# Optimization experiments

Measured on AMD Instinct MI355X. Metric: run time of the kernel, lower is better.

Reference implementation:

```python
import jax, jax.numpy as jnp
import numpy as np

N_HEADS = 16
CONTEXT_WINDOW = 256


def _band_mask(s_q, s_k):
    # True = masked out. Module (causal=True, context_window=256) allows only
    # keys with 0 <= (query_pos - key_pos) < CONTEXT_WINDOW (causal mask is
    # subsumed by the lower band).
    d = jnp.arange(s_q)[:, None] - jnp.arange(s_k)[None, :]
    return ~((d >= 0) & (d < CONTEXT_WINDOW))


def setup_inputs() -> dict:
    key = jax.random.key(0)
    ks = jax.random.split(key, 5)
    B, S, D = 2, 2048, 1024
    std = 0.02
    return {
        "query": jax.random.normal(ks[0], (B, S, D), dtype=jnp.float32),
        "Wq": jax.random.normal(ks[1], (D, D), dtype=jnp.float32) * std,
        "bq": jnp.zeros((D,), dtype=jnp.float32),
        "Wk": jax.random.normal(ks[2], (D, D), dtype=jnp.float32) * std,
        "bk": jnp.zeros((D,), dtype=jnp.float32),
        "Wv": jax.random.normal(ks[3], (D, D), dtype=jnp.float32) * std,
        "bv": jnp.zeros((D,), dtype=jnp.float32),
        "Wo": jax.random.normal(ks[4], (D, D), dtype=jnp.float32) * std,
        "bo": jnp.zeros((D,), dtype=jnp.float32),
    }


def reference(query, Wq, bq, Wk, bk, Wv, bv, Wo, bo):
    B, S, D = query.shape
    H = N_HEADS
    Dh = D // H
    # projections -> [B, H, S, Dh]
    q = (query @ Wq + bq).reshape(B, S, H, Dh).transpose(0, 2, 1, 3)
    k = (query @ Wk + bk).reshape(B, S, H, Dh).transpose(0, 2, 1, 3)
    v = (query @ Wv + bv).reshape(B, S, H, Dh).transpose(0, 2, 1, 3)
    scores = jnp.einsum("bhqd,bhkd->bhqk", q, k) * (1.0 / np.sqrt(Dh))
    mask = _band_mask(S, S)  # [S, S]
    scores = jnp.where(mask[None, None, :, :], -jnp.inf, scores)
    attn = jax.nn.softmax(scores, axis=-1)
    out = jnp.einsum("bhqk,bhkd->bhqd", attn, v)
    out = out.transpose(0, 2, 1, 3).reshape(B, S, D)
    return out @ Wo + bo
```

## Files before the change

kernel.cpp:

```cpp
#include <hip/hip_runtime.h>
#include <hip/hip_bf16.h>


typedef __bf16 bf16x8 __attribute__((ext_vector_type(8)));
typedef float f32x4 __attribute__((ext_vector_type(4)));
typedef short s16x4 __attribute__((ext_vector_type(4)));
typedef unsigned short u16x8 __attribute__((ext_vector_type(8)));
typedef unsigned short u16x4 __attribute__((ext_vector_type(4)));

__device__ __forceinline__ unsigned short f2bf(float f) {
  unsigned int u = __builtin_bit_cast(unsigned int, f);
  u += 0x7FFFu + ((u >> 16) & 1u);
  return (unsigned short)(u >> 16);
}

__device__ __forceinline__ f32x4 mfma32(bf16x8 a, bf16x8 b, f32x4 c) {
  return __builtin_amdgcn_mfma_f32_16x16x32_bf16(a, b, c, 0, 0, 0);
}
__device__ __forceinline__ f32x4 mfma16(s16x4 a, s16x4 b, f32x4 c) {
  return __builtin_amdgcn_mfma_f32_16x16x16bf16_1k(a, b, c, 0, 0, 0);
}

__device__ __forceinline__ void gl16(const unsigned short* gsrc,
                                     unsigned short* lds) {
  __builtin_amdgcn_global_load_lds(
      (const __attribute__((address_space(1))) unsigned int*)gsrc,
      (__attribute__((address_space(3))) unsigned int*)lds, 16, 0, 0);
}

__global__ __launch_bounds__(256) void cvt_all(
    const float* __restrict__ x,
    const float* __restrict__ Wq, const float* __restrict__ Wk,
    const float* __restrict__ Wv, const float* __restrict__ Wo,
    unsigned short* __restrict__ xb, unsigned short* __restrict__ Wt) {
  const int z = blockIdx.z;
  const int tx = threadIdx.x, ty = threadIdx.y;
  if (z == 4) {
    const int tid = (blockIdx.y * 32 + blockIdx.x) * 256 + ty * 32 + tx;
#pragma unroll
    for (int it = 0; it < 4; ++it) {
      const int i = tid + it * 262144;
      const float4 v = ((const float4*)x)[i];
      u16x4 o = { f2bf(v.x), f2bf(v.y), f2bf(v.z), f2bf(v.w) };
      *(u16x4*)(xb + (size_t)i * 4) = o;
    }
    return;
  }
  const float* W = (z == 0) ? Wq : (z == 1) ? Wk : (z == 2) ? Wv : Wo;
  unsigned short* dst = Wt + (size_t)z * 1024 * 1024;
  __shared__ float t[32][33];
  const int n0 = blockIdx.x * 32, k0 = blockIdx.y * 32;
#pragma unroll
  for (int i = 0; i < 32; i += 8)
    t[ty + i][tx] = W[(size_t)(k0 + ty + i) * 1024 + n0 + tx];
  __syncthreads();
#pragma unroll
  for (int i = 0; i < 32; i += 8)
    dst[(size_t)(n0 + ty + i) * 1024 + k0 + tx] = f2bf(t[tx][ty + i]);
}

__global__ __launch_bounds__(256) void gemm_qkv(
    const unsigned short* __restrict__ A, const unsigned short* __restrict__ Bt,
    const float* __restrict__ bq, const float* __restrict__ bk,
    const float* __restrict__ bv,
    unsigned short* __restrict__ q_ws, unsigned short* __restrict__ k_ws,
    unsigned short* __restrict__ v_ws) {
  __shared__ unsigned short Alds[128 * 32];
  __shared__ unsigned short Blds[128 * 32];
  const int tid = threadIdx.x, lane = tid & 63, w = tid >> 6;
  const int lq = lane & 15, lg = lane >> 4;
  const int bm = blockIdx.x, bn = blockIdx.y;
  const int wr = (w >> 1) * 64, wc = (w & 1) * 64;

  const int srow = lane >> 2, scol8 = (lane & 3) * 8;
  const unsigned short* Ag =
      A + (size_t)(bm * 128 + w * 32 + srow) * 1024 + scol8;
  const unsigned short* Bg =
      Bt + (size_t)(bn * 128 + w * 32 + srow) * 1024 + scol8;
  unsigned short* Al0 = Alds + (w * 32) * 32;
  unsigned short* Al1 = Alds + (w * 32 + 16) * 32;
  unsigned short* Bl0 = Blds + (w * 32) * 32;
  unsigned short* Bl1 = Blds + (w * 32 + 16) * 32;

  f32x4 acc[4][4] = {};
  for (int kt = 0; kt < 1024; kt += 32) {
    __syncthreads();
    gl16(Ag + kt, Al0);
    gl16(Ag + kt + 16 * 1024, Al1);
    gl16(Bg + kt, Bl0);
    gl16(Bg + kt + 16 * 1024, Bl1);
    __syncthreads();
    bf16x8 af[4], bfr[4];
#pragma unroll
    for (int m = 0; m < 4; ++m)
      af[m] = *(const bf16x8*)(Alds + (wr + m * 16 + lq) * 32 + lg * 8);
#pragma unroll
    for (int n = 0; n < 4; ++n)
      bfr[n] = *(const bf16x8*)(Blds + (wc + n * 16 + lq) * 32 + lg * 8);
#pragma unroll
    for (int m = 0; m < 4; ++m)
#pragma unroll
      for (int n = 0; n < 4; ++n)
        acc[m][n] = mfma32(af[m], bfr[n], acc[m][n]);
  }

  const int r0 = bm * 128 + wr + lg * 4;
  const int c0g = bn * 128 + wc + lq;
#pragma unroll
  for (int m = 0; m < 4; ++m) {
#pragma unroll
    for (int n = 0; n < 4; ++n) {
      const int col = c0g + n * 16;
#pragma unroll
      for (int j = 0; j < 4; ++j) {
        const int row = r0 + m * 16 + j;
        float v = acc[m][n][j];
        const int t = col >> 10, cc = col & 1023;
        const float* bias = (t == 0) ? bq : ((t == 1) ? bk : bv);
        v += bias[cc];
        if (t == 0) v *= 0.125f;
        unsigned short* dst = (t == 0) ? q_ws : ((t == 1) ? k_ws : v_ws);
        const int h = cc >> 6, dh = cc & 63, b = row >> 11, s = row & 2047;
        dst[((size_t)(b * 16 + h) * 2048 + s) * 64 + dh] = f2bf(v);
      }
    }
  }
}

__global__ __launch_bounds__(256) void gemm_out(
    const unsigned short* __restrict__ A, const unsigned short* __restrict__ Bt,
    const float* __restrict__ bo, float* __restrict__ outp) {
  __shared__ __align__(16) unsigned short Alds[128 * 64];
  __shared__ __align__(16) unsigned short Blds[64 * 64];
  const int tid = threadIdx.x, lane = tid & 63, w = tid >> 6;
  const int lq = lane & 15, lg = lane >> 4;
  const int bm = blockIdx.x, bn = blockIdx.y;
  const int wr = (w >> 1) * 64, wc = (w & 1) * 32;

  const int lrow = lane >> 3;
  const int ksw = (((lane & 7) ^ lrow) << 3);
  const unsigned short* Ag =
      A + (size_t)(bm * 128 + w * 32 + lrow) * 1024 + ksw;
  const unsigned short* Bg =
      Bt + (size_t)(bn * 64 + w * 16 + lrow) * 1024 + ksw;
  unsigned short* AlW = Alds + (w * 32) * 64;
  unsigned short* BlW = Blds + (w * 16) * 64;
  const int cs = lq & 7;

  f32x4 acc[4][2] = {};
  for (int kt = 0; kt < 1024; kt += 64) {
    __syncthreads();
#pragma unroll
    for (int i = 0; i < 4; ++i)
      gl16(Ag + kt + (size_t)i * 8 * 1024, AlW + i * 8 * 64);
#pragma unroll
    for (int i = 0; i < 2; ++i)
      gl16(Bg + kt + (size_t)i * 8 * 1024, BlW + i * 8 * 64);
    __syncthreads();
#pragma unroll
    for (int kk = 0; kk < 2; ++kk) {
      bf16x8 af[4], bfr[2];
#pragma unroll
      for (int m = 0; m < 4; ++m)
        af[m] = *(const bf16x8*)(Alds + (wr + m * 16 + lq) * 64 +
                                 (((kk * 4 + lg) ^ cs) << 3));
#pragma unroll
      for (int n = 0; n < 2; ++n)
        bfr[n] = *(const bf16x8*)(Blds + (wc + n * 16 + lq) * 64 +
                                  (((kk * 4 + lg) ^ cs) << 3));
#pragma unroll
      for (int m = 0; m < 4; ++m)
#pragma unroll
        for (int n = 0; n < 2; ++n)
          acc[m][n] = mfma32(af[m], bfr[n], acc[m][n]);
    }
  }

  const int r0 = bm * 128 + wr + lg * 4;
  const int c0g = bn * 64 + wc + lq;
#pragma unroll
  for (int m = 0; m < 4; ++m)
#pragma unroll
    for (int n = 0; n < 2; ++n) {
      const int col = c0g + n * 16;
#pragma unroll
      for (int j = 0; j < 4; ++j)
        outp[(size_t)(r0 + m * 16 + j) * 1024 + col] = acc[m][n][j] + bo[col];
    }
}

__global__ __launch_bounds__(256) void attn_kernel(
    const unsigned short* __restrict__ q_ws,
    const unsigned short* __restrict__ k_ws,
    const unsigned short* __restrict__ v_ws,
    unsigned short* __restrict__ attn_out) {
  __shared__ unsigned short o_lds[4][16 * 64];
  const int tid = threadIdx.x, lane = tid & 63, w = tid >> 6;
  const int lq = lane & 15, lg = lane >> 4;
  const int bh = blockIdx.y;
  const int q0 = blockIdx.x * 64 + w * 16;
  const unsigned short* Q = q_ws + (size_t)bh * 2048 * 64;
  const unsigned short* Kp = k_ws + (size_t)bh * 2048 * 64;
  const unsigned short* Vp = v_ws + (size_t)bh * 2048 * 64;

  const bf16x8 qf0 = *(const bf16x8*)(Q + (size_t)(q0 + lq) * 64 + lg * 8);
  const bf16x8 qf1 = *(const bf16x8*)(Q + (size_t)(q0 + lq) * 64 + 32 + lg * 8);

  float lsum = 0.f;
  f32x4 oacc[4] = {};
  int t0 = (q0 - 255) >> 4;
  if (t0 < 0) t0 = 0;
  const int t1 = q0 >> 4;

  for (int t = t0; t <= t1; ++t) {
    const int j0 = t * 16;
    const bf16x8 kf0 = *(const bf16x8*)(Kp + (size_t)(j0 + lq) * 64 + lg * 8);
    const bf16x8 kf1 =
        *(const bf16x8*)(Kp + (size_t)(j0 + lq) * 64 + 32 + lg * 8);
    f32x4 stv = {};
    stv = mfma32(kf0, qf0, stv);
    stv = mfma32(kf1, qf1, stv);

    float p[4], ps = 0.f;
#pragma unroll
    for (int r = 0; r < 4; ++r) {
      const int delta = (q0 + lq) - (j0 + lg * 4 + r);
      const bool ok = (delta >= 0) && (delta < 256);
      p[r] = ok ? __expf(stv[r] - 4.0f) : 0.f;
      ps += p[r];
    }
    ps += __shfl_xor(ps, 16);
    ps += __shfl_xor(ps, 32);
    lsum += ps;

    s16x4 pb = { (short)f2bf(p[0]), (short)f2bf(p[1]),
                 (short)f2bf(p[2]), (short)f2bf(p[3]) };
#pragma unroll
    for (int c = 0; c < 4; ++c) {
      s16x4 vf;
#pragma unroll
      for (int j = 0; j < 4; ++j)
        vf[j] = (short)Vp[(size_t)(j0 + lg * 4 + j) * 64 + c * 16 + lq];
      oacc[c] = mfma16(vf, pb, oacc[c]);
    }
  }

  const float rl = 1.f / lsum;
#pragma unroll
  for (int c = 0; c < 4; ++c)
#pragma unroll
    for (int r = 0; r < 4; ++r)
      o_lds[w][lq * 64 + c * 16 + lg * 4 + r] = f2bf(oacc[c][r] * rl);
  __syncthreads();
  const int row = lane >> 2, d0 = (lane & 3) * 16;
  const u16x8 o0 = *(const u16x8*)(&o_lds[w][row * 64 + d0]);
  const u16x8 o1 = *(const u16x8*)(&o_lds[w][row * 64 + d0 + 8]);
  const size_t g =
      ((size_t)((bh >> 4) * 2048 + q0 + row)) * 1024 + (bh & 15) * 64 + d0;
  *(u16x8*)(attn_out + g) = o0;
  *(u16x8*)(attn_out + g + 8) = o1;
}

extern "C" void kernel_launch(void* const* d_in, const int* in_sizes, int n_in,
                              void* d_out, int out_size, void* d_ws,
                              size_t ws_size, hipStream_t stream) {
  const float* query = (const float*)d_in[0];
  const float* Wq = (const float*)d_in[1];
  const float* bq = (const float*)d_in[2];
  const float* Wk = (const float*)d_in[3];
  const float* bk = (const float*)d_in[4];
  const float* Wv = (const float*)d_in[5];
  const float* bv = (const float*)d_in[6];
  const float* Wo = (const float*)d_in[7];
  const float* bo = (const float*)d_in[8];
  float* outp = (float*)d_out;

  char* ws = (char*)d_ws;
  unsigned short* xbf = (unsigned short*)(ws);
  unsigned short* wt  = (unsigned short*)(ws + (8u << 20));
  unsigned short* qws = (unsigned short*)(ws + (16u << 20));
  unsigned short* kws = (unsigned short*)(ws + (24u << 20));
  unsigned short* vws = (unsigned short*)(ws + (32u << 20));

  cvt_all<<<dim3(32, 32, 5), dim3(32, 8), 0, stream>>>(query, Wq, Wk, Wv, Wo,
                                                       xbf, wt);
  gemm_qkv<<<dim3(32, 24), 256, 0, stream>>>(xbf, wt, bq, bk, bv, qws, kws,
                                             vws);
  attn_kernel<<<dim3(32, 32), 256, 0, stream>>>(qws, kws, vws, xbf);
  gemm_out<<<dim3(32, 16), 256, 0, stream>>>(
      xbf, wt + (size_t)3 * 1024 * 1024, bo, outp);
}
```

Measured before the change: 90.93 us.

## Split attention key range across two waves per query strip and combine in LDS

Each block now covers 32 queries instead of 64, and two waves share each 16-query strip, each taking half of the key tiles. The second wave writes its unnormalized partial output and row sums to LDS, and the first wave adds them, normalizes and stores the result. The aim is to halve the serial key loop per wave and double the number of blocks, for more parallelism and latency hiding. The cost is an extra LDS combine, an extra barrier, and more Q loads across blocks. The combine is correct because the softmax uses a fixed offset rather than a running max.

```diff
diff --git a/kernel.cpp b/kernel.cpp
--- a/kernel.cpp
+++ b/kernel.cpp
@@ -194,11 +194,14 @@
     const unsigned short* __restrict__ k_ws,
     const unsigned short* __restrict__ v_ws,
     unsigned short* __restrict__ attn_out) {
-  __shared__ unsigned short o_lds[4][16 * 64];
-  const int tid = threadIdx.x, lane = tid & 63, w = tid >> 6;
+  __shared__ float cmb[2][16 * 65];
+  __shared__ float cmbl[2][16];
+  __shared__ unsigned short o_lds[2][16 * 64];
+  const int tid = threadIdx.x, lane = tid & 63;
+  const int strip = tid >> 7, split = (tid >> 6) & 1;
   const int lq = lane & 15, lg = lane >> 4;
   const int bh = blockIdx.y;
-  const int q0 = blockIdx.x * 64 + w * 16;
+  const int q0 = blockIdx.x * 32 + strip * 16;
   const unsigned short* Q = q_ws + (size_t)bh * 2048 * 64;
   const unsigned short* Kp = k_ws + (size_t)bh * 2048 * 64;
   const unsigned short* Vp = v_ws + (size_t)bh * 2048 * 64;
@@ -211,8 +214,11 @@
   int t0 = (q0 - 255) >> 4;
   if (t0 < 0) t0 = 0;
   const int t1 = q0 >> 4;
-
-  for (int t = t0; t <= t1; ++t) {
+  const int half = (t1 - t0 + 2) >> 1;
+  const int ts = (split == 0) ? t0 : t0 + half;
+  const int te = (split == 0) ? t0 + half - 1 : t1;
+
+  for (int t = ts; t <= te; ++t) {
     const int j0 = t * 16;
     const bf16x8 kf0 = *(const bf16x8*)(Kp + (size_t)(j0 + lq) * 64 + lg * 8);
     const bf16x8 kf1 =
@@ -245,20 +251,35 @@
     }
   }
 
-  const float rl = 1.f / lsum;
-#pragma unroll
-  for (int c = 0; c < 4; ++c)
-#pragma unroll
-    for (int r = 0; r < 4; ++r)
-      o_lds[w][lq * 64 + c * 16 + lg * 4 + r] = f2bf(oacc[c][r] * rl);
+  if (split == 1) {
+#pragma unroll
+    for (int c = 0; c < 4; ++c)
+#pragma unroll
+      for (int r = 0; r < 4; ++r)
+        cmb[strip][lq * 65 + c * 16 + lg * 4 + r] = oacc[c][r];
+    if (lg == 0) cmbl[strip][lq] = lsum;
+  }
   __syncthreads();
-  const int row = lane >> 2, d0 = (lane & 3) * 16;
-  const u16x8 o0 = *(const u16x8*)(&o_lds[w][row * 64 + d0]);
-  const u16x8 o1 = *(const u16x8*)(&o_lds[w][row * 64 + d0 + 8]);
+  if (split == 0) {
+    lsum += cmbl[strip][lq];
+    const float rl = 1.f / lsum;
+#pragma unroll
+    for (int c = 0; c < 4; ++c)
+#pragma unroll
+      for (int r = 0; r < 4; ++r) {
+        const float v =
+            oacc[c][r] + cmb[strip][lq * 65 + c * 16 + lg * 4 + r];
+        o_lds[strip][lq * 64 + c * 16 + lg * 4 + r] = f2bf(v * rl);
+      }
+  }
+  __syncthreads();
+  const int st2 = tid >> 7, stid = tid & 127;
+  const int row = stid >> 3, d0 = (stid & 7) * 8;
+  const int q0s = blockIdx.x * 32 + st2 * 16;
+  const u16x8 ov = *(const u16x8*)(&o_lds[st2][row * 64 + d0]);
   const size_t g =
-      ((size_t)((bh >> 4) * 2048 + q0 + row)) * 1024 + (bh & 15) * 64 + d0;
-  *(u16x8*)(attn_out + g) = o0;
-  *(u16x8*)(attn_out + g + 8) = o1;
+      ((size_t)((bh >> 4) * 2048 + q0s + row)) * 1024 + (bh & 15) * 64 + d0;
+  *(u16x8*)(attn_out + g) = ov;
 }
 
 extern "C" void kernel_launch(void* const* d_in, const int* in_sizes, int n_in,
@@ -286,7 +307,7 @@
                                                        xbf, wt);
   gemm_qkv<<<dim3(32, 24), 256, 0, stream>>>(xbf, wt, bq, bk, bv, qws, kws,
                                              vws);
-  attn_kernel<<<dim3(32, 32), 256, 0, stream>>>(qws, kws, vws, xbf);
+  attn_kernel<<<dim3(64, 32), 256, 0, stream>>>(qws, kws, vws, xbf);
   gemm_out<<<dim3(32, 16), 256, 0, stream>>>(
       xbf, wt + (size_t)3 * 1024 * 1024, bo, outp);
 }
```

Measured after the change: 91.81 us. About the same (+1.0%).
